# Performance work log

Hardware: AMD Instinct MI355X
Metric: run time of the kernel (lower is better)

Reference implementation:

```python
import jax, jax.numpy as jnp
import numpy as np

D = 768; DEPTH = 12; NH = 12; DH = 64; MLP = 3072; P = 16; IMG = 224; HF = 14; FD = 256
B = 2; NV = 4


def _ln(x, g, b):
    m = x.mean(-1, keepdims=True)
    v = ((x - m) ** 2).mean(-1, keepdims=True)
    return (x - m) * jax.lax.rsqrt(v + 1e-6) * g + b


def _vit(x, patch_w, patch_b, cls_tok, pos_emb, blocks, nf_g, nf_b):
    # x: [n,3,224,224] -> tokens [n,197,768] (timm vit_base_patch16_224 forward_features)
    n = x.shape[0]
    p = x.reshape(n, 3, HF, P, HF, P).transpose(0, 2, 4, 1, 3, 5).reshape(n, HF * HF, 3 * P * P)
    tok = p @ patch_w + patch_b
    tok = jnp.concatenate([jnp.broadcast_to(cls_tok, (n, 1, D)), tok], axis=1) + pos_emb

    def block(t, pr):
        l1g, l1b, qw, qb, pw, pb, l2g, l2b, f1w, f1b, f2w, f2b = pr
        h = _ln(t, l1g, l1b)
        qkv = (h @ qw + qb).reshape(n, -1, 3, NH, DH)
        q, k, v = qkv[:, :, 0], qkv[:, :, 1], qkv[:, :, 2]
        att = jax.nn.softmax(jnp.einsum('bqhd,bkhd->bhqk', q, k) / jnp.sqrt(jnp.float32(DH)), axis=-1)
        o = jnp.einsum('bhqk,bkhd->bqhd', att, v).reshape(n, -1, D)
        t = t + o @ pw + pb
        h = _ln(t, l2g, l2b)
        t = t + jax.nn.gelu(h @ f1w + f1b, approximate=False) @ f2w + f2b
        return t, None

    tok, _ = jax.lax.scan(block, tok, blocks)
    return _ln(tok, nf_g, nf_b)


def setup_inputs() -> dict:
    key = jax.random.key(0)
    ks = jax.random.split(key, 24)
    s = 0.02
    imgs = jax.random.normal(ks[0], (B, NV, 3, IMG, IMG), jnp.float32)
    depths = jax.random.uniform(ks[1], (B, NV, IMG, IMG), jnp.float32) * 0.05  # scaled *65.535 -> (0,3.3), inside (0,5)
    t = jax.random.normal(ks[2], (B, NV, 3), jnp.float32) * 0.5
    poses = jnp.broadcast_to(jnp.eye(4, dtype=jnp.float32), (B, NV, 4, 4)).at[:, :, :3, 3].set(t)
    intr = (jnp.zeros((B, NV, 3, 3), jnp.float32)
            .at[:, :, 0, 0].set(200.0).at[:, :, 1, 1].set(200.0)
            .at[:, :, 0, 2].set(112.0).at[:, :, 1, 2].set(112.0).at[:, :, 2, 2].set(1.0))
    grid_points = jax.random.normal(ks[3], (B, 196, 3), jnp.float32)
    d = dict(
        ugv_images=imgs, ugv_depths=depths, camera_poses=poses, intrinsics=intr,
        grid_points_3d=grid_points,
        patch_w=jax.random.normal(ks[4], (3 * P * P, D), jnp.float32) * s,
        patch_b=jnp.zeros((D,), jnp.float32),
        cls_tok=jax.random.normal(ks[5], (1, 1, D), jnp.float32) * s,
        pos_emb=jax.random.normal(ks[6], (1, HF * HF + 1, D), jnp.float32) * s,
        ln1_g=jnp.ones((DEPTH, D), jnp.float32), ln1_b=jnp.zeros((DEPTH, D), jnp.float32),
        qkv_w=jax.random.normal(ks[7], (DEPTH, D, 3 * D), jnp.float32) * s,
        qkv_b=jnp.zeros((DEPTH, 3 * D), jnp.float32),
        proj_w=jax.random.normal(ks[8], (DEPTH, D, D), jnp.float32) * s,
        proj_b=jnp.zeros((DEPTH, D), jnp.float32),
        ln2_g=jnp.ones((DEPTH, D), jnp.float32), ln2_b=jnp.zeros((DEPTH, D), jnp.float32),
        fc1_w=jax.random.normal(ks[9], (DEPTH, D, MLP), jnp.float32) * s,
        fc1_b=jnp.zeros((DEPTH, MLP), jnp.float32),
        fc2_w=jax.random.normal(ks[10], (DEPTH, MLP, D), jnp.float32) * s,
        fc2_b=jnp.zeros((DEPTH, D), jnp.float32),
        nf_g=jnp.ones((D,), jnp.float32), nf_b=jnp.zeros((D,), jnp.float32),
        conv_w=jax.random.normal(ks[11], (FD, D), jnp.float32) * s,
        conv_b=jnp.zeros((FD,), jnp.float32),
    )
    return d


def reference(ugv_images, ugv_depths, camera_poses, intrinsics, grid_points_3d,
              patch_w, patch_b, cls_tok, pos_emb,
              ln1_g, ln1_b, qkv_w, qkv_b, proj_w, proj_b,
              ln2_g, ln2_b, fc1_w, fc1_b, fc2_w, fc2_b,
              nf_g, nf_b, conv_w, conv_b):
    blocks = (ln1_g, ln1_b, qkv_w, qkv_b, proj_w, proj_b, ln2_g, ln2_b, fc1_w, fc1_b, fc2_w, fc2_b)
    tok = _vit(ugv_images.reshape(B * NV, 3, IMG, IMG), patch_w, patch_b, cls_tok, pos_emb, blocks, nf_g, nf_b)
    feats = tok[:, 1:, :].transpose(0, 2, 1).reshape(B, NV, D, HF, HF)  # [B,N,C,Hf,Wf]

    # swap rows 0,1 of w2c, then invert
    w2c = camera_poses[:, :, jnp.array([1, 0, 2, 3]), :]
    c2w = jnp.linalg.inv(w2c)

    d = jax.image.resize(ugv_depths, (B, NV, HF, HF), 'linear', antialias=False) * (65535.0 / 1000.0)
    mask = (d > 0.0) & (d < 5.0)

    fx = intrinsics[:, :, 0, 0][..., None, None]
    fy = intrinsics[:, :, 1, 1][..., None, None]
    cx = intrinsics[:, :, 0, 2][..., None, None]
    cy = intrinsics[:, :, 1, 2][..., None, None]

    u, v = jnp.meshgrid(jnp.arange(HF, dtype=jnp.float32), jnp.arange(HF, dtype=jnp.float32), indexing='xy')
    Xc = -((u - cx) * d / (fx + 1e-8))
    Yc = (v - cy) * d / (fy + 1e-8)
    pts = jnp.stack([Xc, Yc, d, jnp.ones_like(d)], axis=-1)  # [B,N,Hf,Wf,4]
    w = jnp.einsum('bnij,bnhwj->bnhwi', c2w, pts)
    Xw, Yw = w[..., 0], w[..., 1]

    tile = 10.0
    px = Xw * (HF / tile) + HF / 2.0
    py = -(Yw * (HF / tile)) + HF / 2.0
    pxi = jnp.round(px).astype(jnp.int32)
    pyi = jnp.round(py).astype(jnp.int32)
    inb = (pxi >= 0) & (pxi < HF) & (pyi >= 0) & (pyi < HF)
    valid = mask & inb

    HW = HF * HF
    boff = jnp.arange(B, dtype=jnp.int32)[:, None, None, None] * HW
    idx = jnp.where(valid, boff + pyi * HF + pxi, B * HW).reshape(-1)  # invalid -> dummy bucket
    src = feats.transpose(0, 1, 3, 4, 2).reshape(-1, D)  # [B*N*HW, C]
    seg = B * HW + 1

    ssum = jax.ops.segment_sum(src, idx, num_segments=seg)
    cnt = jax.ops.segment_sum(valid.astype(jnp.float32).reshape(-1), idx, num_segments=seg)
    smax = jnp.zeros((seg, D), src.dtype).at[idx].max(src)  # include_self with 0 init, like torch amax

    avg = ssum[:B * HW] / (cnt[:B * HW, None] + 1e-8)
    bev = (avg + smax[:B * HW]) / 2.0
    bev = bev.reshape(B, HF, HF, D)
    out = jnp.einsum('bhwc,oc->bohw', bev, conv_w) + conv_b[None, :, None, None]
    return out
```

## Files before the change

### kernel.cpp

```cpp
#include <hip/hip_runtime.h>
#include <hip/hip_bf16.h>
#include <math.h>
#include <type_traits>
#include <utility>

#define DMODEL 768
#define NTOK 197
#define NIMG 8
#define NHEADS 12
#define MLPD 3072
#define NROWS (NIMG*NTOK)
#define NPATCH (NIMG*196)
#define HF 14
#define BATCH 2
#define NCELL (BATCH*HF*HF)
#define FD 256

typedef __attribute__((ext_vector_type(8))) short s8v;
typedef __attribute__((ext_vector_type(8))) __bf16 b8v;
typedef __attribute__((ext_vector_type(8))) _Float16 h8v;
typedef __attribute__((ext_vector_type(4))) float f32x4;

template <typename V, typename = void>
struct mfma_takes : std::false_type {};
template <typename V>
struct mfma_takes<V, std::void_t<decltype(
    __builtin_amdgcn_mfma_f32_16x16x32_bf16(std::declval<V>(), std::declval<V>(),
                                            std::declval<f32x4>(), 0, 0, 0))>>
    : std::true_type {};

template <typename V>
struct MfmaCall {
    static __device__ inline f32x4 run(s8v a, s8v b, f32x4 c) {
        return __builtin_amdgcn_mfma_f32_16x16x32_bf16(
            __builtin_bit_cast(V, a), __builtin_bit_cast(V, b), c, 0, 0, 0);
    }
};
using mfma_v = std::conditional_t<mfma_takes<b8v>::value, b8v, s8v>;

template <typename V, typename = void>
struct mfma16_takes : std::false_type {};
template <typename V>
struct mfma16_takes<V, std::void_t<decltype(
    __builtin_amdgcn_mfma_f32_16x16x32_f16(std::declval<V>(), std::declval<V>(),
                                           std::declval<f32x4>(), 0, 0, 0))>>
    : std::true_type {};

template <typename V>
struct MfmaF16Call {
    static __device__ inline f32x4 run(s8v a, s8v b, f32x4 c) {
        return __builtin_amdgcn_mfma_f32_16x16x32_f16(
            __builtin_bit_cast(V, a), __builtin_bit_cast(V, b), c, 0, 0, 0);
    }
};
using mfma16_v = std::conditional_t<mfma16_takes<h8v>::value, h8v, s8v>;

typedef __attribute__((address_space(1))) const unsigned int guint_t;
typedef __attribute__((address_space(3))) unsigned int luint_t;

template <int BM, int BN>
__global__ __launch_bounds__(256) void gemm_t(
    const __hip_bfloat16* __restrict__ A, const __hip_bfloat16* __restrict__ BT,
    const float* __restrict__ bias, const float* __restrict__ res,
    void* __restrict__ Cout, int M, int N, int K, int flags, int nx,
    float* __restrict__ part)
{
    constexpr int FM = BM / 32;
    constexpr int FN = BN / 32;
    __shared__ short Asl[BM * 32];
    __shared__ short Bsl[BN * 32];
    int t = threadIdx.x;
    int w = t >> 6, lane = t & 63;

    int nwg = gridDim.x;
    int id = blockIdx.x;
    int q = nwg >> 3, r = nwg & 7;
    int xcd = id & 7;
    int wgid = (xcd < r ? xcd * (q + 1) : r * (q + 1) + (xcd - r) * q) + (id >> 3);
    int bx = wgid % nx, by = wgid / nx;
    int bm = by * BM, bn = bx * BN;

    int S = gridDim.z, z = blockIdx.z;
    int kchunk = K / S;
    int kbeg = z * kchunk, kend = kbeg + kchunk;

    int rbase = (w >> 1) * (BM / 2), cbase = (w & 1) * (BN / 2);

    f32x4 acc[FM][FN];
    #pragma unroll
    for (int i = 0; i < FM; i++)
        #pragma unroll
        for (int j = 0; j < FN; j++)
            acc[i][j] = (f32x4){0.f, 0.f, 0.f, 0.f};

    const short* Ag = (const short*)A;
    const short* Bg = (const short*)BT;

    for (int k0 = kbeg; k0 < kend; k0 += 32) {
        #pragma unroll
        for (int i = 0; i < BM * 4 / 256; i++) {
            int c = i * 256 + t;
            int row = c >> 2, koff = (c & 3) * 8;
            int ga = bm + row; if (ga >= M) ga = M - 1;
            __builtin_amdgcn_global_load_lds(
                (guint_t*)(Ag + (size_t)ga * K + k0 + koff),
                (luint_t*)(Asl + c * 8), 16, 0, 0);
        }
        #pragma unroll
        for (int i = 0; i < BN * 4 / 256; i++) {
            int c = i * 256 + t;
            int row = c >> 2, koff = (c & 3) * 8;
            __builtin_amdgcn_global_load_lds(
                (guint_t*)(Bg + (size_t)(bn + row) * K + k0 + koff),
                (luint_t*)(Bsl + c * 8), 16, 0, 0);
        }
        __syncthreads();

        int kk = (lane >> 4) * 8;
        int rl = lane & 15;
        s8v af[FM], bfr[FN];
        #pragma unroll
        for (int i = 0; i < FM; i++)
            af[i] = *(const s8v*)(Asl + (rbase + i * 16 + rl) * 32 + kk);
        #pragma unroll
        for (int j = 0; j < FN; j++)
            bfr[j] = *(const s8v*)(Bsl + (cbase + j * 16 + rl) * 32 + kk);
        #pragma unroll
        for (int i = 0; i < FM; i++)
            #pragma unroll
            for (int j = 0; j < FN; j++)
                acc[i][j] = MfmaCall<mfma_v>::run(af[i], bfr[j], acc[i][j]);
        __syncthreads();
    }

    int colg = lane & 15;
    int rowg = (lane >> 4) * 4;
    #pragma unroll
    for (int i = 0; i < FM; i++) {
        #pragma unroll
        for (int j = 0; j < FN; j++) {
            #pragma unroll
            for (int qq = 0; qq < 4; qq++) {
                int rr = bm + rbase + i * 16 + rowg + qq;
                int cc = bn + cbase + j * 16 + colg;
                if (rr < M) {
                    float v = acc[i][j][qq];
                    if (flags & 8) {
                        part[((size_t)z * M + rr) * N + cc] = v;
                    } else {
                        if (bias) v += bias[cc];
                        if (flags & 1) v = 0.5f * v * (1.0f + erff(v * 0.7071067811865476f));
                        if (res)  v += res[(size_t)rr * N + cc];
                        if (flags & 2)
                            ((__hip_bfloat16*)Cout)[(size_t)rr * N + cc] = __float2bfloat16(v);
                        else if (flags & 4)
                            ((_Float16*)Cout)[(size_t)rr * N + cc] = (_Float16)v;
                        else
                            ((float*)Cout)[(size_t)rr * N + cc] = v;
                    }
                }
            }
        }
    }
}

template <int NPART, int FINAL>
__global__ __launch_bounds__(256) void redln_kernel(
    const float* __restrict__ part, const float* __restrict__ bias,
    float* __restrict__ tok, const float* __restrict__ g,
    const float* __restrict__ b, __hip_bfloat16* __restrict__ hout,
    float* __restrict__ fout)
{
    int r = blockIdx.x, t = threadIdx.x;
    __shared__ float red[8];
    float v[3];
    #pragma unroll
    for (int i = 0; i < 3; i++) {
        int idx = t + i * 256;
        float x = tok[(size_t)r * DMODEL + idx] + bias[idx];
        x += part[(size_t)r * DMODEL + idx];
        if (NPART == 2) x += part[((size_t)NROWS + r) * DMODEL + idx];
        v[i] = x;
        if (!FINAL) tok[(size_t)r * DMODEL + idx] = x;
    }
    float s = v[0] + v[1] + v[2];
    #pragma unroll
    for (int m = 32; m >= 1; m >>= 1) s += __shfl_xor(s, m);
    int wid = t >> 6, lane = t & 63;
    if (lane == 0) red[wid] = s;
    __syncthreads();
    float mean = (red[0] + red[1] + red[2] + red[3]) * (1.0f / DMODEL);
    float d0 = v[0] - mean, d1 = v[1] - mean, d2 = v[2] - mean;
    float qv = d0 * d0 + d1 * d1 + d2 * d2;
    #pragma unroll
    for (int m = 32; m >= 1; m >>= 1) qv += __shfl_xor(qv, m);
    __syncthreads();
    if (lane == 0) red[4 + wid] = qv;
    __syncthreads();
    float var = (red[4] + red[5] + red[6] + red[7]) * (1.0f / DMODEL);
    float rs = 1.0f / sqrtf(var + 1e-6f);
    float dd[3] = {d0, d1, d2};
    #pragma unroll
    for (int i = 0; i < 3; i++) {
        int idx = t + i * 256;
        float y = dd[i] * rs * g[idx] + b[idx];
        if (FINAL) fout[(size_t)r * DMODEL + idx] = y;
        else       hout[(size_t)r * DMODEL + idx] = __float2bfloat16(y);
    }
}

__global__ __launch_bounds__(256) void assemble_ln_kernel(
    const float* __restrict__ tmp, const float* __restrict__ cls,
    const float* __restrict__ pos, const float* __restrict__ g,
    const float* __restrict__ b, float* __restrict__ tok,
    __hip_bfloat16* __restrict__ hout)
{
    int rr = blockIdx.x;
    int n = rr / NTOK, r = rr % NTOK;
    int t = threadIdx.x;
    __shared__ float red[8];
    float v[3];
    #pragma unroll
    for (int i = 0; i < 3; i++) {
        int idx = t + i * 256;
        float x = (r == 0) ? cls[idx]
                           : tmp[((size_t)n * 196 + r - 1) * DMODEL + idx];
        x += pos[(size_t)r * DMODEL + idx];
        v[i] = x;
        tok[(size_t)rr * DMODEL + idx] = x;
    }
    float s = v[0] + v[1] + v[2];
    #pragma unroll
    for (int m = 32; m >= 1; m >>= 1) s += __shfl_xor(s, m);
    int wid = t >> 6, lane = t & 63;
    if (lane == 0) red[wid] = s;
    __syncthreads();
    float mean = (red[0] + red[1] + red[2] + red[3]) * (1.0f / DMODEL);
    float d0 = v[0] - mean, d1 = v[1] - mean, d2 = v[2] - mean;
    float qv = d0 * d0 + d1 * d1 + d2 * d2;
    #pragma unroll
    for (int m = 32; m >= 1; m >>= 1) qv += __shfl_xor(qv, m);
    __syncthreads();
    if (lane == 0) red[4 + wid] = qv;
    __syncthreads();
    float var = (red[4] + red[5] + red[6] + red[7]) * (1.0f / DMODEL);
    float rs = 1.0f / sqrtf(var + 1e-6f);
    float dd[3] = {d0, d1, d2};
    #pragma unroll
    for (int i = 0; i < 3; i++) {
        int idx = t + i * 256;
        hout[(size_t)rr * DMODEL + idx] = __float2bfloat16(dd[i] * rs * g[idx] + b[idx]);
    }
}

#define AT_STR 232
#define KS_STR 72

__global__ __launch_bounds__(256) void fused_attn_kernel(
    const _Float16* __restrict__ qkv, __hip_bfloat16* __restrict__ O)
{
    __shared__ char smem[29696 + 39168];
    _Float16* Vt = (_Float16*)smem;
    _Float16* Qs = (_Float16*)(smem + 29696);
    _Float16* Ks = Qs + 64 * KS_STR;
    _Float16* Pl = (_Float16*)(smem + 29696);

    int nh = blockIdx.x;
    int n = nh / NHEADS, hh = nh % NHEADS;
    int qoff = blockIdx.y * 64;
    int t = threadIdx.x;
    int w = t >> 6, lane = t & 63;
    int g = lane >> 4, rl = lane & 15;
    const _Float16* base = qkv + (size_t)n * NTOK * 2304;

    for (int idx = t; idx < 208 * 8; idx += 256) {
        int row = idx >> 3, c8 = (idx & 7) * 8;
        if (row < NTOK)
            *(uint4*)(Ks + row * KS_STR + c8) =
                *(const uint4*)(base + (size_t)row * 2304 + 768 + hh * 64 + c8);
        else
            *(uint4*)(Ks + row * KS_STR + c8) = make_uint4(0, 0, 0, 0);
    }
    for (int idx = t; idx < 64 * 8; idx += 256) {
        int row = idx >> 3, c8 = (idx & 7) * 8;
        int gq = qoff + row; if (gq > NTOK - 1) gq = NTOK - 1;
        *(uint4*)(Qs + row * KS_STR + c8) =
            *(const uint4*)(base + (size_t)gq * 2304 + hh * 64 + c8);
    }
    for (int idx = t; idx < NTOK * 8; idx += 256) {
        int k = idx >> 3, dg = (idx & 7) * 8;
        _Float16 tmp[8];
        *(uint4*)tmp = *(const uint4*)(base + (size_t)k * 2304 + 1536 + hh * 64 + dg);
        #pragma unroll
        for (int j = 0; j < 8; j++) Vt[(dg + j) * AT_STR + k] = tmp[j];
    }
    for (int idx = t; idx < 64 * 27; idx += 256) {
        int d = idx / 27, k = NTOK + idx % 27;
        Vt[d * AT_STR + k] = (_Float16)0.f;
    }
    __syncthreads();

    int wq0 = w * 16;
    f32x4 sacc[13];
    #pragma unroll
    for (int tt = 0; tt < 13; tt++) sacc[tt] = (f32x4){0.f, 0.f, 0.f, 0.f};

    #pragma unroll
    for (int s = 0; s < 2; s++) {
        s8v af = *(const s8v*)(Qs + (wq0 + rl) * KS_STR + s * 32 + 8 * g);
        #pragma unroll
        for (int tt = 0; tt < 13; tt++) {
            s8v bf = *(const s8v*)(Ks + (tt * 16 + rl) * KS_STR + s * 32 + 8 * g);
            sacc[tt] = MfmaF16Call<mfma16_v>::run(af, bf, sacc[tt]);
        }
    }
    __syncthreads();

    _Float16* Pw = Pl + wq0 * AT_STR;
    #pragma unroll
    for (int r = 0; r < 4; r++) {
        float vv[13];
        float mx = -3.0e38f;
        #pragma unroll
        for (int tt = 0; tt < 13; tt++) {
            float v = sacc[tt][r] * 0.125f;
            vv[tt] = v;
            if (rl + 16 * tt < NTOK) mx = fmaxf(mx, v);
        }
        mx = fmaxf(mx, __shfl_xor(mx, 1));
        mx = fmaxf(mx, __shfl_xor(mx, 2));
        mx = fmaxf(mx, __shfl_xor(mx, 4));
        mx = fmaxf(mx, __shfl_xor(mx, 8));
        float pv[13];
        float sum = 0.f;
        #pragma unroll
        for (int tt = 0; tt < 13; tt++) {
            float p = (rl + 16 * tt < NTOK) ? __expf(vv[tt] - mx) : 0.f;
            pv[tt] = p; sum += p;
        }
        sum += __shfl_xor(sum, 1);
        sum += __shfl_xor(sum, 2);
        sum += __shfl_xor(sum, 4);
        sum += __shfl_xor(sum, 8);
        float rinv = 1.0f / sum;
        int prow = g * 4 + r;
        #pragma unroll
        for (int tt = 0; tt < 13; tt++)
            Pw[prow * AT_STR + rl + 16 * tt] = (_Float16)(pv[tt] * rinv);
    }
    for (int idx = lane; idx < 16 * 16; idx += 64) {
        int rr = idx >> 4, cc = 208 + (idx & 15);
        Pw[rr * AT_STR + cc] = (_Float16)0.f;
    }

    f32x4 oacc[4];
    #pragma unroll
    for (int j = 0; j < 4; j++) oacc[j] = (f32x4){0.f, 0.f, 0.f, 0.f};

    for (int s = 0; s < 7; s++) {
        s8v pf = *(const s8v*)(Pw + rl * AT_STR + s * 32 + 8 * g);
        s8v vf[4];
        #pragma unroll
        for (int j = 0; j < 4; j++)
            vf[j] = *(const s8v*)(Vt + (j * 16 + rl) * AT_STR + s * 32 + 8 * g);
        #pragma unroll
        for (int j = 0; j < 4; j++)
            oacc[j] = MfmaF16Call<mfma16_v>::run(pf, vf[j], oacc[j]);
    }

    #pragma unroll
    for (int j = 0; j < 4; j++) {
        #pragma unroll
        for (int r = 0; r < 4; r++) {
            int qidx = qoff + wq0 + g * 4 + r;
            if (qidx < NTOK) {
                int d = j * 16 + rl;
                O[((size_t)n * NTOK + qidx) * DMODEL + hh * 64 + d] =
                    __float2bfloat16(oacc[j][r]);
            }
        }
    }
}

__device__ inline void transpose_tile(const float* __restrict__ src,
                                      __hip_bfloat16* __restrict__ dst,
                                      int K, int N, int b)
{
    __shared__ float tl[32][33];
    int nt = N >> 5;
    int n0 = (b % nt) * 32, k0 = (b / nt) * 32;
    int tx = threadIdx.x & 31, ty = threadIdx.x >> 5;
    #pragma unroll
    for (int i = 0; i < 4; i++)
        tl[ty + i * 8][tx] = src[(size_t)(k0 + ty + i * 8) * N + n0 + tx];
    __syncthreads();
    #pragma unroll
    for (int i = 0; i < 4; i++)
        dst[(size_t)(n0 + ty + i * 8) * K + k0 + tx] = __float2bfloat16(tl[tx][ty + i * 8]);
}

__global__ __launch_bounds__(256) void convT_all(
    const float* __restrict__ qkv_w, const float* __restrict__ proj_w,
    const float* __restrict__ fc1_w, const float* __restrict__ fc2_w,
    const float* __restrict__ patch_w,
    __hip_bfloat16* __restrict__ wbuf, __hip_bfloat16* __restrict__ patchT)
{
    int b = blockIdx.x;
    if (b < 82944) {
        int layer = b / 6912, rem = b % 6912;
        __hip_bfloat16* wl = wbuf + (size_t)layer * 7077888;
        const float* src; __hip_bfloat16* dst; int K, N, tb;
        if (rem < 1728)      { tb = rem;        src = qkv_w  + (size_t)layer * 768 * 2304; dst = wl;           K = 768;  N = 2304; }
        else if (rem < 2304) { tb = rem - 1728; src = proj_w + (size_t)layer * 768 * 768;  dst = wl + 1769472; K = 768;  N = 768;  }
        else if (rem < 4608) { tb = rem - 2304; src = fc1_w  + (size_t)layer * 768 * 3072; dst = wl + 2359296; K = 768;  N = 3072; }
        else                 { tb = rem - 4608; src = fc2_w  + (size_t)layer * 3072 * 768; dst = wl + 4718592; K = 3072; N = 768;  }
        transpose_tile(src, dst, K, N, tb);
    } else {
        transpose_tile(patch_w, patchT, 768, 768, b - 82944);
    }
}

__global__ __launch_bounds__(256) void patch_extract_kernel(
    const float* __restrict__ img, __hip_bfloat16* __restrict__ Pm)
{
    size_t e = (size_t)blockIdx.x * 256 + threadIdx.x;
    if (e >= (size_t)NPATCH * DMODEL) return;
    int cidx = (int)(e % DMODEL);
    int r    = (int)(e / DMODEL);
    int n  = r / 196, s = r % 196;
    int hi = s / HF, wi = s % HF;
    int c  = cidx >> 8, py = (cidx >> 4) & 15, px = cidx & 15;
    Pm[e] = __float2bfloat16(
        img[(((size_t)n * 3 + c) * 224 + hi * 16 + py) * 224 + wi * 16 + px]);
}

__device__ void invert4(const float m[16], float out[16]) {
    float inv[16];
    inv[0] = m[5]*m[10]*m[15] - m[5]*m[11]*m[14] - m[9]*m[6]*m[15] + m[9]*m[7]*m[14] + m[13]*m[6]*m[11] - m[13]*m[7]*m[10];
    inv[4] = -m[4]*m[10]*m[15] + m[4]*m[11]*m[14] + m[8]*m[6]*m[15] - m[8]*m[7]*m[14] - m[12]*m[6]*m[11] + m[12]*m[7]*m[10];
    inv[8] = m[4]*m[9]*m[15] - m[4]*m[11]*m[13] - m[8]*m[5]*m[15] + m[8]*m[7]*m[13] + m[12]*m[5]*m[11] - m[12]*m[7]*m[9];
    inv[12] = -m[4]*m[9]*m[14] + m[4]*m[10]*m[13] + m[8]*m[5]*m[14] - m[8]*m[6]*m[13] - m[12]*m[5]*m[10] + m[12]*m[6]*m[9];
    inv[1] = -m[1]*m[10]*m[15] + m[1]*m[11]*m[14] + m[9]*m[2]*m[15] - m[9]*m[3]*m[14] - m[13]*m[2]*m[11] + m[13]*m[3]*m[10];
    inv[5] = m[0]*m[10]*m[15] - m[0]*m[11]*m[14] - m[8]*m[2]*m[15] + m[8]*m[3]*m[14] + m[12]*m[2]*m[11] - m[12]*m[3]*m[10];
    inv[9] = -m[0]*m[9]*m[15] + m[0]*m[11]*m[13] + m[8]*m[1]*m[15] - m[8]*m[3]*m[13] - m[12]*m[1]*m[11] + m[12]*m[3]*m[9];
    inv[13] = m[0]*m[9]*m[14] - m[0]*m[10]*m[13] - m[8]*m[1]*m[14] + m[8]*m[2]*m[13] + m[12]*m[1]*m[10] - m[12]*m[2]*m[9];
    inv[2] = m[1]*m[6]*m[15] - m[1]*m[7]*m[14] - m[5]*m[2]*m[15] + m[5]*m[3]*m[14] + m[13]*m[2]*m[7] - m[13]*m[3]*m[6];
    inv[6] = -m[0]*m[6]*m[15] + m[0]*m[7]*m[14] + m[4]*m[2]*m[15] - m[4]*m[3]*m[14] - m[12]*m[2]*m[7] + m[12]*m[3]*m[6];
    inv[10] = m[0]*m[5]*m[15] - m[0]*m[7]*m[13] - m[4]*m[1]*m[15] + m[4]*m[3]*m[13] + m[12]*m[1]*m[7] - m[12]*m[3]*m[5];
    inv[14] = -m[0]*m[5]*m[14] + m[0]*m[6]*m[13] + m[4]*m[1]*m[14] - m[4]*m[2]*m[13] - m[12]*m[1]*m[6] + m[12]*m[2]*m[5];
    inv[3] = -m[1]*m[6]*m[11] + m[1]*m[7]*m[10] + m[5]*m[2]*m[11] - m[5]*m[3]*m[10] - m[9]*m[2]*m[7] + m[9]*m[3]*m[6];
    inv[7] = m[0]*m[6]*m[11] - m[0]*m[7]*m[10] - m[4]*m[2]*m[11] + m[4]*m[3]*m[10] + m[8]*m[2]*m[7] - m[8]*m[3]*m[6];
    inv[11] = -m[0]*m[5]*m[11] + m[0]*m[7]*m[9] + m[4]*m[1]*m[11] - m[4]*m[3]*m[9] - m[8]*m[1]*m[7] + m[8]*m[3]*m[5];
    inv[15] = m[0]*m[5]*m[10] - m[0]*m[6]*m[9] - m[4]*m[1]*m[10] + m[4]*m[2]*m[9] + m[8]*m[1]*m[6] - m[8]*m[2]*m[5];
    float det = m[0]*inv[0] + m[1]*inv[4] + m[2]*inv[8] + m[3]*inv[12];
    det = 1.0f / det;
    for (int i = 0; i < 16; i++) out[i] = inv[i] * det;
}

__global__ __launch_bounds__(256) void bev_index_kernel(
    const float* __restrict__ depths, const float* __restrict__ poses,
    const float* __restrict__ intr, int* __restrict__ idxbuf)
{
    int bv = blockIdx.x;
    int b  = bv / 4;
    __shared__ float c2w[16];
    if (threadIdx.x == 0) {
        float w2c[16];
        const float* Pm = poses + bv * 16;
        const int perm[4] = {1, 0, 2, 3};
        for (int i = 0; i < 4; i++)
            for (int j = 0; j < 4; j++)
                w2c[i * 4 + j] = Pm[perm[i] * 4 + j];
        invert4(w2c, c2w);
    }
    __syncthreads();
    int t = threadIdx.x;
    if (t >= 196) return;
    int hh = t / HF, ww = t % HF;
    const float* dp = depths + (size_t)bv * 224 * 224;
    int r0 = hh * 16 + 7, c0 = ww * 16 + 7;
    float d = 0.25f * (dp[r0 * 224 + c0] + dp[r0 * 224 + c0 + 1] +
                       dp[(r0 + 1) * 224 + c0] + dp[(r0 + 1) * 224 + c0 + 1]);
    d *= 65.535f;
    bool mask = (d > 0.0f) && (d < 5.0f);
    float fx = intr[bv * 9 + 0], fy = intr[bv * 9 + 4];
    float cx = intr[bv * 9 + 2], cy = intr[bv * 9 + 5];
    float u = (float)ww, v = (float)hh;
    float Xc = -((u - cx) * d / (fx + 1e-8f));
    float Yc = (v - cy) * d / (fy + 1e-8f);
    float Xw = c2w[0] * Xc + c2w[1] * Yc + c2w[2] * d + c2w[3];
    float Yw = c2w[4] * Xc + c2w[5] * Yc + c2w[6] * d + c2w[7];
    float px = Xw * 1.4f + 7.0f;
    float py = -(Yw * 1.4f) + 7.0f;
    int pxi = (int)rintf(px);
    int pyi = (int)rintf(py);
    bool inb = (pxi >= 0) && (pxi < HF) && (pyi >= 0) && (pyi < HF);
    idxbuf[bv * 196 + t] = (mask && inb) ? (b * 196 + pyi * HF + pxi) : -1;
}

__global__ __launch_bounds__(256) void splat_kernel(
    const float* __restrict__ src, const int* __restrict__ idxbuf,
    float* __restrict__ ssum, float* __restrict__ smax, float* __restrict__ cnt)
{
    int r = blockIdx.x;
    int idx = idxbuf[r];
    if (idx < 0) return;
    int bv = r / 196, s = r % 196;
    const float* row = src + ((size_t)bv * NTOK + 1 + s) * DMODEL;
    int t = threadIdx.x;
    for (int d = t; d < DMODEL; d += 256) {
        float v = row[d];
        atomicAdd(&ssum[(size_t)idx * DMODEL + d], v);
        atomicMax((int*)(smax + (size_t)idx * DMODEL + d), __float_as_int(v));
    }
    if (t == 0) atomicAdd(&cnt[idx], 1.0f);
}

__global__ __launch_bounds__(256) void bev_conv_kernel(
    const float* __restrict__ ssum, const float* __restrict__ smax,
    const float* __restrict__ cnt, const float* __restrict__ convw,
    const float* __restrict__ convb, float* __restrict__ out)
{
    int cell = blockIdx.x;
    __shared__ float bev[DMODEL];
    int t = threadIdx.x;
    float c = cnt[cell];
    for (int d = t; d < DMODEL; d += 256)
        bev[d] = 0.5f * (ssum[(size_t)cell * DMODEL + d] / (c + 1e-8f) +
                         smax[(size_t)cell * DMODEL + d]);
    __syncthreads();
    float acc = convb[t];
    const float4* wr = (const float4*)(convw + (size_t)t * DMODEL);
    #pragma unroll 4
    for (int dc = 0; dc < DMODEL / 4; dc++) {
        float4 w4 = wr[dc];
        acc += bev[dc * 4 + 0] * w4.x + bev[dc * 4 + 1] * w4.y +
               bev[dc * 4 + 2] * w4.z + bev[dc * 4 + 3] * w4.w;
    }
    int b = cell / 196, s = cell % 196;
    out[((size_t)b * FD + t) * 196 + s] = acc;
}

extern "C" void kernel_launch(void* const* d_in, const int* in_sizes, int n_in,
                              void* d_out, int out_size, void* d_ws, size_t ws_size,
                              hipStream_t stream) {
    const float* imgs    = (const float*)d_in[0];
    const float* depths  = (const float*)d_in[1];
    const float* poses   = (const float*)d_in[2];
    const float* intr    = (const float*)d_in[3];
    const float* patch_w = (const float*)d_in[5];
    const float* patch_b = (const float*)d_in[6];
    const float* cls_tok = (const float*)d_in[7];
    const float* pos_emb = (const float*)d_in[8];
    const float* ln1_g   = (const float*)d_in[9];
    const float* ln1_b   = (const float*)d_in[10];
    const float* qkv_w   = (const float*)d_in[11];
    const float* qkv_b   = (const float*)d_in[12];
    const float* proj_w  = (const float*)d_in[13];
    const float* proj_b  = (const float*)d_in[14];
    const float* ln2_g   = (const float*)d_in[15];
    const float* ln2_b   = (const float*)d_in[16];
    const float* fc1_w   = (const float*)d_in[17];
    const float* fc1_b   = (const float*)d_in[18];
    const float* fc2_w   = (const float*)d_in[19];
    const float* fc2_b   = (const float*)d_in[20];
    const float* nf_g    = (const float*)d_in[21];
    const float* nf_b    = (const float*)d_in[22];
    const float* conv_w  = (const float*)d_in[23];
    const float* conv_b  = (const float*)d_in[24];
    float* out = (float*)d_out;
    float* ws  = (float*)d_ws;

    const size_t OFF_TOK  = 0;
    const size_t OFF_FB   = 1210368;
    const size_t OFF_PB   = 3631104;
    const size_t OFF_HB   = 6051840;
    const size_t OFF_PT   = 6657024;
    const size_t OFF_SSUM = 6951936;
    const size_t OFF_SMAX = 7252992;
    const size_t OFF_CNT  = 7554048;
    const size_t OFF_IDX  = 7554560;
    const size_t OFF_W    = 7556608;

    float* tok  = ws + OFF_TOK;
    float* fbig = ws + OFF_FB;
    float* pbuf = ws + OFF_PB;
    _Float16* qkv_h = (_Float16*)pbuf;
    __hip_bfloat16* hb  = (__hip_bfloat16*)(ws + OFF_HB);
    __hip_bfloat16* pT  = (__hip_bfloat16*)(ws + OFF_PT);
    __hip_bfloat16* wbuf = (__hip_bfloat16*)(ws + OFF_W);
    float* ssum = ws + OFF_SSUM;
    float* smax = ws + OFF_SMAX;
    float* cnt  = ws + OFF_CNT;
    int*   idxb = (int*)(ws + OFF_IDX);

    const int MT = (NROWS + 63) / 64;
    const int MTP = (NPATCH + 63) / 64;

    convT_all<<<83520, 256, 0, stream>>>(qkv_w, proj_w, fc1_w, fc2_w, patch_w, wbuf, pT);

    patch_extract_kernel<<<(NPATCH * DMODEL) / 256, 256, 0, stream>>>(imgs, hb);
    gemm_t<64, 64><<<dim3(12 * MTP, 1, 1), 256, 0, stream>>>(
        hb, pT, patch_b, nullptr, fbig, NPATCH, 768, 768, 0, 12, nullptr);
    assemble_ln_kernel<<<NROWS, 256, 0, stream>>>(
        fbig, cls_tok, pos_emb, ln1_g, ln1_b, tok, hb);

    for (int l = 0; l < 12; l++) {
        __hip_bfloat16* wl  = wbuf + (size_t)l * 7077888;
        __hip_bfloat16* wq  = wl;
        __hip_bfloat16* wp  = wl + 1769472;
        __hip_bfloat16* wf1 = wl + 2359296;
        __hip_bfloat16* wf2 = wl + 4718592;

        gemm_t<64, 128><<<dim3(18 * MT, 1, 1), 256, 0, stream>>>(
            hb, wq, qkv_b + (size_t)l * 2304, nullptr, qkv_h, NROWS, 2304, 768,
            4 , 18, nullptr);
        fused_attn_kernel<<<dim3(NIMG * NHEADS, 4), 256, 0, stream>>>(qkv_h, hb);
        gemm_t<64, 64><<<dim3(12 * MT, 1, 1), 256, 0, stream>>>(
            hb, wp, nullptr, nullptr, nullptr, NROWS, 768, 768,
            8 , 12, fbig);
        redln_kernel<1, 0><<<NROWS, 256, 0, stream>>>(
            fbig, proj_b + (size_t)l * DMODEL, tok,
            ln2_g + l * DMODEL, ln2_b + l * DMODEL, hb, nullptr);
        gemm_t<64, 128><<<dim3(24 * MT, 1, 1), 256, 0, stream>>>(
            hb, wf1, fc1_b + (size_t)l * MLPD, nullptr, pbuf, NROWS, 3072, 768,
            3 , 24, nullptr);
        gemm_t<64, 64><<<dim3(12 * MT, 1, 2), 256, 0, stream>>>(
            (__hip_bfloat16*)pbuf, wf2, nullptr, nullptr, nullptr, NROWS, 768, 3072,
            8 , 12, fbig);
        if (l < 11) {
            redln_kernel<2, 0><<<NROWS, 256, 0, stream>>>(
                fbig, fc2_b + (size_t)l * DMODEL, tok,
                ln1_g + (l + 1) * DMODEL, ln1_b + (l + 1) * DMODEL, hb, nullptr);
        } else {
            redln_kernel<2, 1><<<NROWS, 256, 0, stream>>>(
                fbig, fc2_b + (size_t)l * DMODEL, tok,
                nf_g, nf_b, nullptr, pbuf);
        }
    }

    bev_index_kernel<<<NIMG, 256, 0, stream>>>(depths, poses, intr, idxb);
    hipMemsetAsync(ssum, 0, (2 * (size_t)NCELL * DMODEL + 512) * sizeof(float), stream);
    splat_kernel<<<NPATCH, 256, 0, stream>>>(pbuf, idxb, ssum, smax, cnt);

    bev_conv_kernel<<<NCELL, 256, 0, stream>>>(ssum, smax, cnt, conv_w, conv_b, out);
}
```

Baseline: 1.681 ms.

## Double-buffer GEMM LDS tiles, widen weight transpose tiles, split-K proj GEMM

The GEMM now uses two LDS buffers so the next K-slice's global-to-LDS loads are issued before the current slice's MFMAs, leaving one barrier per iteration. The weight-conversion kernel moves to 64x32 tiles with 16-byte vectorized bf16 stores, which halves the block count. The projection GEMM is split over K into two partial sums, reduced by redln<2>, to put more workgroups in flight. Risks are twice the LDS per block, which can lower occupancy, and extra partial-sum traffic for the projection.

```diff
diff --git a/kernel.cpp b/kernel.cpp
--- a/kernel.cpp
+++ b/kernel.cpp
@@ -67,8 +67,8 @@
 {
     constexpr int FM = BM / 32;
     constexpr int FN = BN / 32;
-    __shared__ short Asl[BM * 32];
-    __shared__ short Bsl[BN * 32];
+    __shared__ short Asl[2][BM * 32];
+    __shared__ short Bsl[2][BN * 32];
     int t = threadIdx.x;
     int w = t >> 6, lane = t & 63;
 
@@ -82,7 +82,8 @@
 
     int S = gridDim.z, z = blockIdx.z;
     int kchunk = K / S;
-    int kbeg = z * kchunk, kend = kbeg + kchunk;
+    int kbeg = z * kchunk;
+    int nk = kchunk >> 5;
 
     int rbase = (w >> 1) * (BM / 2), cbase = (w & 1) * (BN / 2);
 
@@ -96,7 +97,7 @@
     const short* Ag = (const short*)A;
     const short* Bg = (const short*)BT;
 
-    for (int k0 = kbeg; k0 < kend; k0 += 32) {
+    auto STAGE = [&](int buf, int k0) {
         #pragma unroll
         for (int i = 0; i < BM * 4 / 256; i++) {
             int c = i * 256 + t;
@@ -104,7 +105,7 @@
             int ga = bm + row; if (ga >= M) ga = M - 1;
             __builtin_amdgcn_global_load_lds(
                 (guint_t*)(Ag + (size_t)ga * K + k0 + koff),
-                (luint_t*)(Asl + c * 8), 16, 0, 0);
+                (luint_t*)(&Asl[buf][0] + c * 8), 16, 0, 0);
         }
         #pragma unroll
         for (int i = 0; i < BN * 4 / 256; i++) {
@@ -112,25 +113,30 @@
             int row = c >> 2, koff = (c & 3) * 8;
             __builtin_amdgcn_global_load_lds(
                 (guint_t*)(Bg + (size_t)(bn + row) * K + k0 + koff),
-                (luint_t*)(Bsl + c * 8), 16, 0, 0);
-        }
+                (luint_t*)(&Bsl[buf][0] + c * 8), 16, 0, 0);
+        }
+    };
+
+    STAGE(0, kbeg);
+    int kk = (lane >> 4) * 8;
+    int rl = lane & 15;
+
+    for (int kt = 0; kt < nk; kt++) {
+        int cur = kt & 1;
         __syncthreads();
-
-        int kk = (lane >> 4) * 8;
-        int rl = lane & 15;
+        if (kt + 1 < nk) STAGE(cur ^ 1, kbeg + (kt + 1) * 32);
         s8v af[FM], bfr[FN];
         #pragma unroll
         for (int i = 0; i < FM; i++)
-            af[i] = *(const s8v*)(Asl + (rbase + i * 16 + rl) * 32 + kk);
+            af[i] = *(const s8v*)(&Asl[cur][0] + (rbase + i * 16 + rl) * 32 + kk);
         #pragma unroll
         for (int j = 0; j < FN; j++)
-            bfr[j] = *(const s8v*)(Bsl + (cbase + j * 16 + rl) * 32 + kk);
+            bfr[j] = *(const s8v*)(&Bsl[cur][0] + (cbase + j * 16 + rl) * 32 + kk);
         #pragma unroll
         for (int i = 0; i < FM; i++)
             #pragma unroll
             for (int j = 0; j < FN; j++)
                 acc[i][j] = MfmaCall<mfma_v>::run(af[i], bfr[j], acc[i][j]);
-        __syncthreads();
     }
 
     int colg = lane & 15;
@@ -382,21 +388,26 @@
     }
 }
 
-__device__ inline void transpose_tile(const float* __restrict__ src,
-                                      __hip_bfloat16* __restrict__ dst,
-                                      int K, int N, int b)
-{
-    __shared__ float tl[32][33];
-    int nt = N >> 5;
-    int n0 = (b % nt) * 32, k0 = (b / nt) * 32;
-    int tx = threadIdx.x & 31, ty = threadIdx.x >> 5;
-    #pragma unroll
-    for (int i = 0; i < 4; i++)
-        tl[ty + i * 8][tx] = src[(size_t)(k0 + ty + i * 8) * N + n0 + tx];
-    __syncthreads();
-    #pragma unroll
-    for (int i = 0; i < 4; i++)
-        dst[(size_t)(n0 + ty + i * 8) * K + k0 + tx] = __float2bfloat16(tl[tx][ty + i * 8]);
+__device__ inline void transpose_tile64(const float* __restrict__ src,
+                                        __hip_bfloat16* __restrict__ dst,
+                                        int K, int N, int b)
+{
+    __shared__ float tl[64][33];
+    int ntn = N >> 5;
+    int n0 = (b % ntn) * 32, k0 = (b / ntn) * 64;
+    int t = threadIdx.x;
+    #pragma unroll
+    for (int i = 0; i < 8; i++) {
+        int idx = i * 256 + t;
+        int kk = idx >> 5, nn = idx & 31;
+        tl[kk][nn] = src[(size_t)(k0 + kk) * N + n0 + nn];
+    }
+    __syncthreads();
+    int n = t >> 3, kc = t & 7;
+    __hip_bfloat16 v[8];
+    #pragma unroll
+    for (int j = 0; j < 8; j++) v[j] = __float2bfloat16(tl[kc * 8 + j][n]);
+    *(uint4*)(dst + (size_t)(n0 + n) * K + k0 + kc * 8) = *(uint4*)v;
 }
 
 __global__ __launch_bounds__(256) void convT_all(
@@ -406,17 +417,17 @@
     __hip_bfloat16* __restrict__ wbuf, __hip_bfloat16* __restrict__ patchT)
 {
     int b = blockIdx.x;
-    if (b < 82944) {
-        int layer = b / 6912, rem = b % 6912;
+    if (b < 41472) {
+        int layer = b / 3456, rem = b % 3456;
         __hip_bfloat16* wl = wbuf + (size_t)layer * 7077888;
         const float* src; __hip_bfloat16* dst; int K, N, tb;
-        if (rem < 1728)      { tb = rem;        src = qkv_w  + (size_t)layer * 768 * 2304; dst = wl;           K = 768;  N = 2304; }
-        else if (rem < 2304) { tb = rem - 1728; src = proj_w + (size_t)layer * 768 * 768;  dst = wl + 1769472; K = 768;  N = 768;  }
-        else if (rem < 4608) { tb = rem - 2304; src = fc1_w  + (size_t)layer * 768 * 3072; dst = wl + 2359296; K = 768;  N = 3072; }
-        else                 { tb = rem - 4608; src = fc2_w  + (size_t)layer * 3072 * 768; dst = wl + 4718592; K = 3072; N = 768;  }
-        transpose_tile(src, dst, K, N, tb);
+        if (rem < 864)       { tb = rem;        src = qkv_w  + (size_t)layer * 768 * 2304; dst = wl;           K = 768;  N = 2304; }
+        else if (rem < 1152) { tb = rem - 864;  src = proj_w + (size_t)layer * 768 * 768;  dst = wl + 1769472; K = 768;  N = 768;  }
+        else if (rem < 2304) { tb = rem - 1152; src = fc1_w  + (size_t)layer * 768 * 3072; dst = wl + 2359296; K = 768;  N = 3072; }
+        else                 { tb = rem - 2304; src = fc2_w  + (size_t)layer * 3072 * 768; dst = wl + 4718592; K = 3072; N = 768;  }
+        transpose_tile64(src, dst, K, N, tb);
     } else {
-        transpose_tile(patch_w, patchT, 768, 768, b - 82944);
+        transpose_tile64(patch_w, patchT, 768, 768, b - 41472);
     }
 }
 
@@ -597,7 +608,7 @@
     const int MT = (NROWS + 63) / 64;
     const int MTP = (NPATCH + 63) / 64;
 
-    convT_all<<<83520, 256, 0, stream>>>(qkv_w, proj_w, fc1_w, fc2_w, patch_w, wbuf, pT);
+    convT_all<<<41760, 256, 0, stream>>>(qkv_w, proj_w, fc1_w, fc2_w, patch_w, wbuf, pT);
 
     patch_extract_kernel<<<(NPATCH * DMODEL) / 256, 256, 0, stream>>>(imgs, hb);
     gemm_t<64, 64><<<dim3(12 * MTP, 1, 1), 256, 0, stream>>>(
@@ -616,10 +627,10 @@
             hb, wq, qkv_b + (size_t)l * 2304, nullptr, qkv_h, NROWS, 2304, 768,
             4 , 18, nullptr);
         fused_attn_kernel<<<dim3(NIMG * NHEADS, 4), 256, 0, stream>>>(qkv_h, hb);
-        gemm_t<64, 64><<<dim3(12 * MT, 1, 1), 256, 0, stream>>>(
+        gemm_t<64, 64><<<dim3(12 * MT, 1, 2), 256, 0, stream>>>(
             hb, wp, nullptr, nullptr, nullptr, NROWS, 768, 768,
             8 , 12, fbig);
-        redln_kernel<1, 0><<<NROWS, 256, 0, stream>>>(
+        redln_kernel<2, 0><<<NROWS, 256, 0, stream>>>(
             fbig, proj_b + (size_t)l * DMODEL, tok,
             ln2_g + l * DMODEL, ln2_b + l * DMODEL, hb, nullptr);
         gemm_t<64, 128><<<dim3(24 * MT, 1, 1), 256, 0, stream>>>(
```

After: 1.584 ms. 5.8% less time.
